# Kernel tuning notes

Measured on AMD Instinct MI355X. Metric: run time of the kernel, lower is better.

## Reference

```python
import jax, jax.numpy as jnp
import numpy as np

SIGMA = 1.0
ALPHA = 1.5
EPS = 1e-08
N, D = 8192, 128


def setup_inputs() -> dict:
    key = jax.random.key(0)
    k1, k2 = jax.random.split(key)
    z1 = jax.random.normal(k1, (N, D), dtype=jnp.float32)
    z2 = jax.random.normal(k2, (N, D), dtype=jnp.float32)
    return {"z1": z1, "z2": z2}


def _l2_normalize(x, eps=1e-12):
    # matches F.normalize(x, dim=1): x / max(||x||, eps)
    n = jnp.linalg.norm(x, axis=1, keepdims=True)
    return x / jnp.maximum(n, eps)


def _f_prime(u):
    # KL divergence: f'(u) = log(u + eps) + 1
    return jnp.log(u + EPS) + 1.0


def _f_star(t):
    # KL divergence conjugate: f*(t) = exp(t - 1)
    return jnp.exp(t - 1.0)


def reference(z1, z2):
    z1 = _l2_normalize(z1)
    z2 = _l2_normalize(z2)
    n = z1.shape[0]

    # positive term: ||z1_i - z2_i||^2 per row
    d_pos = jnp.sum((z1 - z2) ** 2, axis=1)                       # (N,)
    g_pos = jnp.exp(-d_pos / (2.0 * SIGMA ** 2))
    s_pos = _f_prime(g_pos)

    # negative term: squared pairwise distances within z1 (N x N)
    sq = jnp.sum(z1 * z1, axis=1)                                  # (N,)
    d2 = sq[:, None] + sq[None, :] - 2.0 * (z1 @ z1.T)             # (N, N)
    d2 = jnp.maximum(d2, 0.0)
    g_neg = jnp.exp(-d2 / (2.0 * SIGMA ** 2))
    s_neg = _f_prime(g_neg)
    star_neg = _f_star(s_neg)

    # masked mean over off-diagonal entries (N*(N-1) of them)
    off_diag = 1.0 - jnp.eye(n, dtype=star_neg.dtype)
    star_mean = jnp.sum(star_neg * off_diag) / (n * (n - 1))

    loss = -jnp.mean(s_pos) + ALPHA * star_mean
    return loss
```

## Files before the change

kernel.cpp:

```cpp
#include <hip/hip_runtime.h>

#define NROWS 8192
#define DIM 128
#define NT 64
#define NPAIRBLK (NT * (NT + 1) / 2)

typedef _Float16 f16x8 __attribute__((ext_vector_type(8)));
typedef _Float16 f16x2 __attribute__((ext_vector_type(2)));
typedef float f32x16 __attribute__((ext_vector_type(16)));

#define L2E 1.4426950408889634f

#define AS1(p) ((const __attribute__((address_space(1))) void*)(p))
#define AS3(p) ((__attribute__((address_space(3))) void*)(p))

__global__ __launch_bounds__(1024) void fmicl_normalize(
    const float* __restrict__ z1, const float* __restrict__ z2,
    _Float16* __restrict__ zh, float* __restrict__ sposB) {
  const int wid = threadIdx.x >> 6;
  const int lane = threadIdx.x & 63;
  const int row = blockIdx.x * 16 + wid;
  const float2 a = ((const float2*)(z1 + (size_t)row * DIM))[lane];
  const float2 b = ((const float2*)(z2 + (size_t)row * DIM))[lane];
  float s1 = a.x * a.x + a.y * a.y;
  float s2 = b.x * b.x + b.y * b.y;
#pragma unroll
  for (int off = 32; off; off >>= 1) {
    s1 += __shfl_xor(s1, off);
    s2 += __shfl_xor(s2, off);
  }
  const float inv1 = 1.0f / fmaxf(sqrtf(s1), 1e-12f);
  const float inv2 = 1.0f / fmaxf(sqrtf(s2), 1e-12f);
  const float n1x = a.x * inv1, n1y = a.y * inv1;
  const float n2x = b.x * inv2, n2y = b.y * inv2;
  const float dx = n1x - n2x, dy = n1y - n2y;
  float dp = dx * dx + dy * dy;
#pragma unroll
  for (int off = 32; off; off >>= 1) dp += __shfl_xor(dp, off);
  f16x2 h;
  h.x = (_Float16)n1x;
  h.y = (_Float16)n1y;
  *(f16x2*)(zh + (size_t)row * DIM + 2 * lane) = h;
  __shared__ float sposL[16];
  if (lane == 0)
    sposL[wid] = logf(expf(-0.5f * dp) + 1e-8f) + 1.0f;
  __syncthreads();
  if (threadIdx.x == 0) {
    float s = 0.0f;
#pragma unroll
    for (int k = 0; k < 16; ++k) s += sposL[k];
    sposB[blockIdx.x] = s;
  }
}

__global__ __launch_bounds__(512, 4) void fmicl_pairwise(
    const _Float16* __restrict__ zh, float* __restrict__ pairP) {
  __shared__ _Float16 S[256 * DIM];
  __shared__ float wsum[8];

  const int tid = threadIdx.x;
  const int tile = (blockIdx.x & 7) * (NPAIRBLK / 8) + (blockIdx.x >> 3);

  int rt = (int)(64.5f - sqrtf(64.5f * 64.5f - 2.0f * (float)tile));
  if (rt < 0) rt = 0;
  while (rt > 0 && (rt * NT - (rt * (rt - 1)) / 2) > tile) --rt;
  while (((rt + 1) * NT - ((rt + 1) * rt) / 2) <= tile) ++rt;
  const int ct = rt + (tile - (rt * NT - (rt * (rt - 1)) / 2));

  const int lane = tid & 63;
  const int wid = tid >> 6;
  const int i0 = rt << 7;
  const int j0 = ct << 7;

#pragma unroll
  for (int t = 0; t < 8; ++t) {
    const int P = t * 8 + wid;
    const int R = P * 4 + (lane >> 4);
    const int csrc = (lane & 15) ^ (R & 15);
    const _Float16* srow = (R < 128) ? zh + (size_t)(i0 + R) * DIM
                                     : zh + (size_t)(j0 + R - 128) * DIM;
    __builtin_amdgcn_global_load_lds(AS1(srow + csrc * 8), AS3(S + P * 512),
                                     16, 0, 0);
  }
  __syncthreads();

  const int l31 = lane & 31;
  const int lhi = lane >> 5;
  const int wm = (wid >> 1) * 32;
  const int wn = (wid & 1) * 64;
  const uint4* S4 = (const uint4*)S;
  const int ra = wm + l31;
  const int rb0 = 128 + wn + l31;
  const int rb1 = 128 + wn + 32 + l31;
  f32x16 acc0 = {}, acc1 = {};
#pragma unroll
  for (int ks = 0; ks < 8; ++ks) {
    const int kg = ks * 2 + lhi;
    const uint4 va = S4[ra * 16 + (kg ^ (ra & 15))];
    const uint4 vb0 = S4[rb0 * 16 + (kg ^ (rb0 & 15))];
    const uint4 vb1 = S4[rb1 * 16 + (kg ^ (rb1 & 15))];
    const f16x8 af = __builtin_bit_cast(f16x8, va);
    acc0 = __builtin_amdgcn_mfma_f32_32x32x16_f16(
        af, __builtin_bit_cast(f16x8, vb0), acc0, 0, 0, 0);
    acc1 = __builtin_amdgcn_mfma_f32_32x32x16_f16(
        af, __builtin_bit_cast(f16x8, vb1), acc1, 0, 0, 0);
  }

  float gsum = 0.0f;
#pragma unroll
  for (int ni = 0; ni < 2; ++ni) {
    const f32x16& acc = ni ? acc1 : acc0;
    const bool diagsub = (rt == ct) && (wm == wn + ni * 32);
    if (diagsub) {
#pragma unroll
      for (int r = 0; r < 16; ++r) {
        const float e = __builtin_amdgcn_exp2f(fmaf(L2E, acc[r], -L2E));
        const int mloc = (r & 3) + 4 * lhi + 8 * (r >> 2);
        gsum += (mloc != l31) ? e : 0.0f;
      }
    } else {
#pragma unroll
      for (int r = 0; r < 16; ++r)
        gsum += __builtin_amdgcn_exp2f(fmaf(L2E, acc[r], -L2E));
    }
  }
#pragma unroll
  for (int off = 32; off; off >>= 1) gsum += __shfl_xor(gsum, off);
  if (lane == 0) wsum[wid] = gsum;
  __syncthreads();
  if (tid == 0) {
    float s = 0.0f;
#pragma unroll
    for (int k = 0; k < 8; ++k) s += wsum[k];
    pairP[tile] = (rt == ct) ? s : 2.0f * s;
  }
}

__global__ void fmicl_reduce(const float* __restrict__ pairP,
                             const float* __restrict__ sposB,
                             float* __restrict__ out) {
  const int t = threadIdx.x;
  double nsum = (double)pairP[t] + (double)pairP[t + 1024];
  if (t < NPAIRBLK - 2048) nsum += (double)pairP[t + 2048];
  double psum = (t < 512) ? (double)sposB[t] : 0.0;
#pragma unroll
  for (int off = 32; off; off >>= 1) {
    nsum += __shfl_xor(nsum, off);
    psum += __shfl_xor(psum, off);
  }
  __shared__ double ls[2][16];
  const int lane = t & 63;
  const int wid = t >> 6;
  if (lane == 0) {
    ls[0][wid] = nsum;
    ls[1][wid] = psum;
  }
  __syncthreads();
  if (t == 0) {
    double n = 0.0, p = 0.0;
#pragma unroll
    for (int k = 0; k < 16; ++k) {
      n += ls[0][k];
      p += ls[1][k];
    }
    const double pos_mean = p / (double)NROWS;
    const double star_mean = n / ((double)NROWS * (double)(NROWS - 1)) + 1e-8;
    out[0] = (float)(-pos_mean + 1.5 * star_mean);
  }
}

extern "C" void kernel_launch(void* const* d_in, const int* in_sizes, int n_in,
                              void* d_out, int out_size, void* d_ws,
                              size_t ws_size, hipStream_t stream) {
  const float* z1 = (const float*)d_in[0];
  const float* z2 = (const float*)d_in[1];
  float* out = (float*)d_out;
  char* ws = (char*)d_ws;

  float* pairP = (float*)(ws + 0);
  float* sposB = (float*)(ws + 8448);
  _Float16* zh = (_Float16*)(ws + 10496);

  fmicl_normalize<<<512, 1024, 0, stream>>>(z1, z2, zh, sposB);
  fmicl_pairwise<<<NPAIRBLK, 512, 0, stream>>>(zh, pairP);
  fmicl_reduce<<<1, 1024, 0, stream>>>(pairP, sposB, out);
}
```

Baseline: 30.13 us.

## Process chunks of four column tiles per block with register-held A and double-buffered B

```diff
diff --git a/kernel.cpp b/kernel.cpp
--- a/kernel.cpp
+++ b/kernel.cpp
@@ -3,7 +3,8 @@
 #define NROWS 8192
 #define DIM 128
 #define NT 64
-#define NPAIRBLK (NT * (NT + 1) / 2)
+#define NCHUNK 544
+#define CHUNK 4
 
 typedef _Float16 f16x8 __attribute__((ext_vector_type(8)));
 typedef _Float16 f16x2 __attribute__((ext_vector_type(2)));
@@ -53,77 +54,125 @@
   }
 }
 
+__device__ __forceinline__ void stageB(const _Float16* __restrict__ zh,
+                                       _Float16* buf, int ct, int wid,
+                                       int lane) {
+  const _Float16* base = zh + ((size_t)ct << 7) * DIM;
+#pragma unroll
+  for (int it = 0; it < 4; ++it) {
+    const int P = it * 8 + wid;
+    const int R = P * 4 + (lane >> 4);
+    const int cs = (lane & 15) ^ (R & 15);
+    __builtin_amdgcn_global_load_lds(AS1(base + (size_t)R * DIM + cs * 8),
+                                     AS3(buf + P * 512), 16, 0, 0);
+  }
+}
+
 __global__ __launch_bounds__(512, 4) void fmicl_pairwise(
     const _Float16* __restrict__ zh, float* __restrict__ pairP) {
-  __shared__ _Float16 S[256 * DIM];
+  __shared__ _Float16 B0[128 * DIM];
+  __shared__ _Float16 B1[128 * DIM];
   __shared__ float wsum[8];
 
   const int tid = threadIdx.x;
-  const int tile = (blockIdx.x & 7) * (NPAIRBLK / 8) + (blockIdx.x >> 3);
-
-  int rt = (int)(64.5f - sqrtf(64.5f * 64.5f - 2.0f * (float)tile));
-  if (rt < 0) rt = 0;
-  while (rt > 0 && (rt * NT - (rt * (rt - 1)) / 2) > tile) --rt;
-  while (((rt + 1) * NT - ((rt + 1) * rt) / 2) <= tile) ++rt;
-  const int ct = rt + (tile - (rt * NT - (rt * (rt - 1)) / 2));
-
   const int lane = tid & 63;
   const int wid = tid >> 6;
-  const int i0 = rt << 7;
-  const int j0 = ct << 7;
-
-#pragma unroll
-  for (int t = 0; t < 8; ++t) {
-    const int P = t * 8 + wid;
-    const int R = P * 4 + (lane >> 4);
-    const int csrc = (lane & 15) ^ (R & 15);
-    const _Float16* srow = (R < 128) ? zh + (size_t)(i0 + R) * DIM
-                                     : zh + (size_t)(j0 + R - 128) * DIM;
-    __builtin_amdgcn_global_load_lds(AS1(srow + csrc * 8), AS3(S + P * 512),
-                                     16, 0, 0);
-  }
-  __syncthreads();
+
+  const int c = (blockIdx.x & 7) * (NCHUNK / 8) + (blockIdx.x >> 3);
+
+  int rt = 0, accum = 0;
+#pragma unroll 1
+  for (; rt < 64; ++rt) {
+    const int nc = (64 - rt + 3) >> 2;
+    if (c < accum + nc) break;
+    accum += nc;
+  }
+  const int k = c - accum;
+  const int ct0 = rt + k * CHUNK;
+  const int len = min(CHUNK, 64 - ct0);
 
   const int l31 = lane & 31;
   const int lhi = lane >> 5;
-  const int wm = (wid >> 1) * 32;
-  const int wn = (wid & 1) * 64;
-  const uint4* S4 = (const uint4*)S;
-  const int ra = wm + l31;
-  const int rb0 = 128 + wn + l31;
-  const int rb1 = 128 + wn + 32 + l31;
-  f32x16 acc0 = {}, acc1 = {};
-#pragma unroll
-  for (int ks = 0; ks < 8; ++ks) {
-    const int kg = ks * 2 + lhi;
-    const uint4 va = S4[ra * 16 + (kg ^ (ra & 15))];
-    const uint4 vb0 = S4[rb0 * 16 + (kg ^ (rb0 & 15))];
-    const uint4 vb1 = S4[rb1 * 16 + (kg ^ (rb1 & 15))];
-    const f16x8 af = __builtin_bit_cast(f16x8, va);
-    acc0 = __builtin_amdgcn_mfma_f32_32x32x16_f16(
-        af, __builtin_bit_cast(f16x8, vb0), acc0, 0, 0, 0);
-    acc1 = __builtin_amdgcn_mfma_f32_32x32x16_f16(
-        af, __builtin_bit_cast(f16x8, vb1), acc1, 0, 0, 0);
-  }
+  const int m = wid >> 2;
+  const int n = wid & 3;
+  const int i0 = rt << 7;
+
+  uint4 areg0[8], areg1[8];
+  {
+    const uint4* r0 = (const uint4*)(zh + (size_t)(i0 + m * 64 + l31) * DIM);
+    const uint4* r1 = r0 + 32 * (DIM / 8);
+#pragma unroll
+    for (int ks = 0; ks < 8; ++ks) {
+      areg0[ks] = r0[2 * ks + lhi];
+      areg1[ks] = r1[2 * ks + lhi];
+    }
+  }
+
+  stageB(zh, B0, ct0, wid, lane);
 
   float gsum = 0.0f;
-#pragma unroll
-  for (int ni = 0; ni < 2; ++ni) {
-    const f32x16& acc = ni ? acc1 : acc0;
-    const bool diagsub = (rt == ct) && (wm == wn + ni * 32);
-    if (diagsub) {
-#pragma unroll
-      for (int r = 0; r < 16; ++r) {
-        const float e = __builtin_amdgcn_exp2f(fmaf(L2E, acc[r], -L2E));
-        const int mloc = (r & 3) + 4 * lhi + 8 * (r >> 2);
-        gsum += (mloc != l31) ? e : 0.0f;
+#pragma unroll 1
+  for (int t = 0; t < len; ++t) {
+    _Float16* curB = (t & 1) ? B1 : B0;
+    if (t + 1 < len) {
+      stageB(zh, (t & 1) ? B0 : B1, ct0 + t + 1, wid, lane);
+      asm volatile("s_waitcnt vmcnt(4)" ::: "memory");
+    } else {
+      asm volatile("s_waitcnt vmcnt(0)" ::: "memory");
+    }
+    __builtin_amdgcn_s_barrier();
+    __builtin_amdgcn_sched_barrier(0);
+
+    const uint4* B4 = (const uint4*)curB;
+    const int rb = n * 32 + l31;
+    f32x16 a0 = {}, a1 = {};
+#pragma unroll
+    for (int ks = 0; ks < 8; ++ks) {
+      const uint4 vb = B4[rb * 16 + ((2 * ks + lhi) ^ (rb & 15))];
+      const f16x8 bf = __builtin_bit_cast(f16x8, vb);
+      a0 = __builtin_amdgcn_mfma_f32_32x32x16_f16(
+          __builtin_bit_cast(f16x8, areg0[ks]), bf, a0, 0, 0, 0);
+      a1 = __builtin_amdgcn_mfma_f32_32x32x16_f16(
+          __builtin_bit_cast(f16x8, areg1[ks]), bf, a1, 0, 0, 0);
+    }
+
+    const int ct = ct0 + t;
+    float tsum = 0.0f;
+    {
+      const bool dsub = (ct == rt) && (n == 2 * m);
+      if (dsub) {
+#pragma unroll
+        for (int r = 0; r < 16; ++r) {
+          const float e = __builtin_amdgcn_exp2f(fmaf(L2E, a0[r], -L2E));
+          const int mloc = (r & 3) + 4 * lhi + 8 * (r >> 2);
+          tsum += (mloc != l31) ? e : 0.0f;
+        }
+      } else {
+#pragma unroll
+        for (int r = 0; r < 16; ++r)
+          tsum += __builtin_amdgcn_exp2f(fmaf(L2E, a0[r], -L2E));
       }
-    } else {
-#pragma unroll
-      for (int r = 0; r < 16; ++r)
-        gsum += __builtin_amdgcn_exp2f(fmaf(L2E, acc[r], -L2E));
-    }
-  }
+    }
+    {
+      const bool dsub = (ct == rt) && (n == 2 * m + 1);
+      if (dsub) {
+#pragma unroll
+        for (int r = 0; r < 16; ++r) {
+          const float e = __builtin_amdgcn_exp2f(fmaf(L2E, a1[r], -L2E));
+          const int mloc = (r & 3) + 4 * lhi + 8 * (r >> 2);
+          tsum += (mloc != l31) ? e : 0.0f;
+        }
+      } else {
+#pragma unroll
+        for (int r = 0; r < 16; ++r)
+          tsum += __builtin_amdgcn_exp2f(fmaf(L2E, a1[r], -L2E));
+      }
+    }
+    gsum += (ct == rt) ? tsum : (tsum + tsum);
+
+    __builtin_amdgcn_s_barrier();
+  }
+
 #pragma unroll
   for (int off = 32; off; off >>= 1) gsum += __shfl_xor(gsum, off);
   if (lane == 0) wsum[wid] = gsum;
@@ -131,8 +180,8 @@
   if (tid == 0) {
     float s = 0.0f;
 #pragma unroll
-    for (int k = 0; k < 8; ++k) s += wsum[k];
-    pairP[tile] = (rt == ct) ? s : 2.0f * s;
+    for (int q = 0; q < 8; ++q) s += wsum[q];
+    pairP[c] = s;
   }
 }
 
@@ -140,8 +189,7 @@
                              const float* __restrict__ sposB,
                              float* __restrict__ out) {
   const int t = threadIdx.x;
-  double nsum = (double)pairP[t] + (double)pairP[t + 1024];
-  if (t < NPAIRBLK - 2048) nsum += (double)pairP[t + 2048];
+  double nsum = (t < NCHUNK) ? (double)pairP[t] : 0.0;
   double psum = (t < 512) ? (double)sposB[t] : 0.0;
 #pragma unroll
   for (int off = 32; off; off >>= 1) {
@@ -157,14 +205,14 @@
   }
   __syncthreads();
   if (t == 0) {
-    double n = 0.0, p = 0.0;
-#pragma unroll
-    for (int k = 0; k < 16; ++k) {
-      n += ls[0][k];
-      p += ls[1][k];
-    }
-    const double pos_mean = p / (double)NROWS;
-    const double star_mean = n / ((double)NROWS * (double)(NROWS - 1)) + 1e-8;
+    double nn = 0.0, pp = 0.0;
+#pragma unroll
+    for (int q = 0; q < 16; ++q) {
+      nn += ls[0][q];
+      pp += ls[1][q];
+    }
+    const double pos_mean = pp / (double)NROWS;
+    const double star_mean = nn / ((double)NROWS * (double)(NROWS - 1)) + 1e-8;
     out[0] = (float)(-pos_mean + 1.5 * star_mean);
   }
 }
@@ -178,10 +226,10 @@
   char* ws = (char*)d_ws;
 
   float* pairP = (float*)(ws + 0);
-  float* sposB = (float*)(ws + 8448);
-  _Float16* zh = (_Float16*)(ws + 10496);
+  float* sposB = (float*)(ws + 4096);
+  _Float16* zh = (_Float16*)(ws + 6144);
 
   fmicl_normalize<<<512, 1024, 0, stream>>>(z1, z2, zh, sposB);
-  fmicl_pairwise<<<NPAIRBLK, 512, 0, stream>>>(zh, pairP);
+  fmicl_pairwise<<<NCHUNK, 512, 0, stream>>>(zh, pairP);
   fmicl_reduce<<<1, 1024, 0, stream>>>(pairP, sposB, out);
 }
```

Result: slower. 42.88 us (+42.3%).
